# Performance work log

Hardware: AMD Instinct MI355X
Metric: run time of the kernel (lower is better)

The kernel has to match this reference:

```python
import jax, jax.numpy as jnp
import numpy as np
from math import sqrt

N_HEAD = 8
N_GROUPS = 32
EPS = 1e-5


def setup_inputs() -> dict:
    key = jax.random.key(0)
    k1, k2, k3 = jax.random.split(key, 3)
    B, C, T = 4, 256, 2048
    x = jax.random.normal(k1, (B, C, T), dtype=jnp.float32)
    gn_w = jnp.ones((C,), dtype=jnp.float32)
    gn_b = jnp.zeros((C,), dtype=jnp.float32)
    qkv_w = jax.random.normal(k2, (3 * C, C), dtype=jnp.float32) * (1.0 / sqrt(C))
    out_w = jax.random.normal(k3, (C, C), dtype=jnp.float32) * (1.0 / sqrt(C))
    out_b = jnp.zeros((C,), dtype=jnp.float32)
    return {"x": x, "gn_w": gn_w, "gn_b": gn_b, "qkv_w": qkv_w, "out_w": out_w, "out_b": out_b}


def reference(x, gn_w, gn_b, qkv_w, out_w, out_b):
    B, C, T = x.shape
    H = N_HEAD
    D = C // H
    # GroupNorm over (C//G, T) within each of G groups
    xg = x.reshape(B, N_GROUPS, -1)
    mu = jnp.mean(xg, axis=-1, keepdims=True)
    var = jnp.mean(jnp.square(xg - mu), axis=-1, keepdims=True)
    norm = ((xg - mu) * jax.lax.rsqrt(var + EPS)).reshape(B, C, T)
    norm = norm * gn_w[:, None] + gn_b[:, None]
    # 1x1 conv QKV projection (no bias)
    qkv = jnp.einsum('oc,bct->bot', qkv_w, norm)  # [B, 3C, T]
    qkv = qkv.reshape(B, H, 3 * D, T)
    q, k, v = jnp.split(qkv, 3, axis=2)  # each [B, H, D, T]
    # note: scale uses full channel count, matching the original module
    attn = jnp.einsum('bncl,bncx->bnlx', q, k) / sqrt(C)  # [B, H, T, T]
    attn = jax.nn.softmax(attn, axis=-1)
    out = jnp.einsum('bnlx,bncx->bncl', attn, v).reshape(B, C, T)
    # 1x1 conv out projection (with bias)
    out = jnp.einsum('oc,bct->bot', out_w, out) + out_b[:, None]
    return out + x
```

## Files before the change

kernel.cpp:

```cpp
#include <hip/hip_runtime.h>
#include <hip/hip_bf16.h>

#define B_ 4
#define C_ 256
#define T_ 2048
#define H_ 8

typedef __attribute__((ext_vector_type(8))) short short8;
typedef __attribute__((ext_vector_type(4))) float floatx4;
typedef __attribute__((ext_vector_type(16))) float floatx16;

static __device__ __forceinline__ float b2f(ushort u) {
  union { float f; unsigned v; } w; w.v = ((unsigned)u) << 16; return w.f;
}
static __device__ __forceinline__ ushort f2b(float f) {
  __hip_bfloat16 h = __float2bfloat16(f);
  return *reinterpret_cast<ushort*>(&h);
}

#define QWS_OFF   0
#define OWS_OFF   196608
#define OBS_OFF   262144
#define WCONV_N   262400
#define STATS_OFF 262400
#define NP_OFF    262912
#define QT_OFF    2360064
#define KT_OFF    4457216
#define VP_OFF    6554368
#define AT_OFF    8651520

__global__ __launch_bounds__(256) void prep_k(
    const void* __restrict__ xraw, const void* __restrict__ qw,
    const void* __restrict__ ow, const void* __restrict__ ob,
    const unsigned* __restrict__ gwraw, float* __restrict__ stats,
    ushort* __restrict__ ws)
{
  const bool f32 = (gwraw[0] == 0x3F800000u);
  const int tid = threadIdx.x;
  if (blockIdx.x >= 128) {
    const int idx = (blockIdx.x - 128) * 256 + tid;
    if (idx >= WCONV_N) return;
    if (idx < OWS_OFF) {
      const float v = f32 ? ((const float*)qw)[idx] : b2f(((const ushort*)qw)[idx]);
      const int o = idx >> 8, c = idx & 255;
      ws[QWS_OFF + ((size_t)(c >> 5) * 768 + o) * 32 + (c & 31)] = f2b(v);
    } else if (idx < OBS_OFF) {
      const int li = idx - OWS_OFF;
      const float v = f32 ? ((const float*)ow)[li] : b2f(((const ushort*)ow)[li]);
      const int o = li >> 8, c = li & 255;
      ws[OWS_OFF + ((size_t)(c >> 5) * 256 + o) * 32 + (c & 31)] = f2b(v);
    } else {
      const int li = idx - OBS_OFF;
      const float v = f32 ? ((const float*)ob)[li] : b2f(((const ushort*)ob)[li]);
      ws[OBS_OFF + li] = f2b(v);
    }
    return;
  }
  const int bg = blockIdx.x;
  const size_t base = (size_t)bg * 8 * T_;
  float s = 0.f, ss = 0.f;
  if (f32) {
    const float4* xv = (const float4*)((const float*)xraw + base);
    for (int i = tid; i < 4096; i += 256) {
      float4 u = xv[i];
      s += u.x + u.y + u.z + u.w;
      ss += u.x * u.x + u.y * u.y + u.z * u.z + u.w * u.w;
    }
  } else {
    const uint4* xv = (const uint4*)((const ushort*)xraw + base);
    for (int i = tid; i < 2048; i += 256) {
      uint4 u = xv[i];
      unsigned w4[4] = {u.x, u.y, u.z, u.w};
#pragma unroll
      for (int j = 0; j < 4; ++j) {
        float a = b2f((ushort)(w4[j] & 0xffff));
        float c = b2f((ushort)(w4[j] >> 16));
        s += a + c; ss += a * a + c * c;
      }
    }
  }
  __shared__ float sh[512];
  sh[tid] = s; sh[256 + tid] = ss;
  __syncthreads();
  for (int st = 128; st > 0; st >>= 1) {
    if (tid < st) { sh[tid] += sh[tid + st]; sh[256 + tid] += sh[256 + tid + st]; }
    __syncthreads();
  }
  if (tid == 0) {
    float mu = sh[0] * (1.f / 16384.f);
    float var = sh[256] * (1.f / 16384.f) - mu * mu;
    stats[bg * 2] = mu;
    stats[bg * 2 + 1] = rsqrtf(var + 1e-5f);
  }
}

__global__ __launch_bounds__(256) void gnapply_k(
    const void* __restrict__ xraw, const unsigned* __restrict__ gwraw,
    const void* __restrict__ gbraw, const float* __restrict__ stats,
    ushort* __restrict__ np)
{
  const bool f32 = (gwraw[0] == 0x3F800000u);
  const int t0 = blockIdx.x * 16, b = blockIdx.y;
  const int tid = threadIdx.x;
  __shared__ ushort lt[16][264];

  if (f32) {
    const int tl = tid & 15;
    const int cb = tid >> 4;
#pragma unroll
    for (int pass = 0; pass < 16; ++pass) {
      const int c = pass * 16 + cb;
      const int g = c >> 3;
      const float mu = stats[(b * 32 + g) * 2];
      const float rs = stats[(b * 32 + g) * 2 + 1];
      const float wv = ((const float*)gwraw)[c] * rs;
      const float bv = ((const float*)gbraw)[c] - mu * wv;
      const float xv = ((const float*)xraw)[((size_t)b * C_ + c) * T_ + t0 + tl];
      lt[tl][c] = f2b(xv * wv + bv);
    }
  } else {
    const int tl = (tid & 7) * 2;
    const int cb = tid >> 3;
#pragma unroll
    for (int pass = 0; pass < 8; ++pass) {
      const int c = pass * 32 + cb;
      const int g = c >> 3;
      const float mu = stats[(b * 32 + g) * 2];
      const float rs = stats[(b * 32 + g) * 2 + 1];
      const float wv = b2f(((const ushort*)gwraw)[c]) * rs;
      const float bv = b2f(((const ushort*)gbraw)[c]) - mu * wv;
      const unsigned u = *(const unsigned*)((const ushort*)xraw +
                          ((size_t)b * C_ + c) * T_ + t0 + tl);
      lt[tl][c]     = f2b(b2f((ushort)(u & 0xffff)) * wv + bv);
      lt[tl + 1][c] = f2b(b2f((ushort)(u >> 16)) * wv + bv);
    }
  }
  __syncthreads();
  {
    const int t = tid >> 4, ci = (tid & 15) * 8;
#pragma unroll
    for (int half = 0; half < 2; ++half) {
      const int c = half * 128 + ci;
      const int kp = c >> 5, co = c & 31;
      uint4 v = *(const uint4*)&lt[t][c];
      *(uint4*)(np + (((size_t)b * 8 + kp) * T_ + t0 + t) * 32 + co) = v;
    }
  }
}

__global__ __launch_bounds__(256) void qkvgemm_k(
    const ushort* __restrict__ qwp, const ushort* __restrict__ np,
    ushort* __restrict__ qt, ushort* __restrict__ kt, ushort* __restrict__ vP)
{
  const int b = blockIdx.z;
  const int m0 = blockIdx.x * 32;
  const int h = blockIdx.x / 3, sec = blockIdx.x % 3;
  const int tid = threadIdx.x;
  const int wave = tid >> 6, lane = tid & 63;
  const int qlane = lane & 15, quad = lane >> 4;
  const int tw0 = blockIdx.y * 128 + wave * 32;
  const float qscale = 0.0625f * 1.4426950408889634f;

  floatx4 acc[2][2] = {};
  if (sec < 2) {
#pragma unroll
    for (int k0 = 0; k0 < C_; k0 += 32) {
      const int kp = k0 >> 5;
      short8 af[2], bf[2];
#pragma unroll
      for (int mi = 0; mi < 2; ++mi)
        af[mi] = *(const short8*)(np + (((size_t)b * 8 + kp) * T_ + tw0 + mi * 16 + qlane) * 32 + quad * 8);
#pragma unroll
      for (int ni = 0; ni < 2; ++ni)
        bf[ni] = *(const short8*)(qwp + ((size_t)kp * 768 + m0 + ni * 16 + qlane) * 32 + quad * 8);
#pragma unroll
      for (int mi = 0; mi < 2; ++mi)
#pragma unroll
        for (int ni = 0; ni < 2; ++ni)
          acc[mi][ni] = __builtin_amdgcn_mfma_f32_16x16x32_bf16(af[mi], bf[ni], acc[mi][ni], 0, 0, 0);
    }
    const float sc = (sec == 0) ? qscale : 1.f;
    ushort* dst = ((sec == 0) ? qt : kt) + (size_t)(b * H_ + h) * T_ * 32;
#pragma unroll
    for (int mi = 0; mi < 2; ++mi)
#pragma unroll
      for (int ni = 0; ni < 2; ++ni)
#pragma unroll
        for (int r = 0; r < 4; ++r) {
          const int t = tw0 + mi * 16 + quad * 4 + r;
          const int d = ni * 16 + qlane;
          dst[(size_t)t * 32 + d] = f2b(acc[mi][ni][r] * sc);
        }
  } else {
#pragma unroll
    for (int k0 = 0; k0 < C_; k0 += 32) {
      const int kp = k0 >> 5;
      short8 af[2], bf[2];
#pragma unroll
      for (int mi = 0; mi < 2; ++mi)
        af[mi] = *(const short8*)(qwp + ((size_t)kp * 768 + m0 + mi * 16 + qlane) * 32 + quad * 8);
#pragma unroll
      for (int ni = 0; ni < 2; ++ni)
        bf[ni] = *(const short8*)(np + (((size_t)b * 8 + kp) * T_ + tw0 + ni * 16 + qlane) * 32 + quad * 8);
#pragma unroll
      for (int mi = 0; mi < 2; ++mi)
#pragma unroll
        for (int ni = 0; ni < 2; ++ni)
          acc[mi][ni] = __builtin_amdgcn_mfma_f32_16x16x32_bf16(af[mi], bf[ni], acc[mi][ni], 0, 0, 0);
    }
    ushort* dst = vP + (((size_t)(b * H_ + h) * 64 + (tw0 >> 5)) * 32) * 32;
#pragma unroll
    for (int mi = 0; mi < 2; ++mi)
#pragma unroll
      for (int ni = 0; ni < 2; ++ni)
#pragma unroll
        for (int r = 0; r < 4; ++r) {
          const int d = mi * 16 + quad * 4 + r;
          const int xi = ni * 16 + qlane;
          dst[(size_t)d * 32 + xi] = f2b(acc[mi][ni][r]);
        }
  }
}

__global__ __launch_bounds__(256) void attn_k(
    const ushort* __restrict__ qt, const ushort* __restrict__ kt,
    const ushort* __restrict__ vP, ushort* __restrict__ att)
{
  const int bh = blockIdx.y;
  const int tid = threadIdx.x;
  const int wave = tid >> 6, lane = tid & 63;
  const int qlane = lane & 15, quad = lane >> 4;
  const int l32 = lane & 31, hl = lane >> 5;
  const int l0 = blockIdx.x * 32;

  const ushort* qp = qt + (size_t)bh * T_ * 32;
  const ushort* kp = kt + (size_t)bh * T_ * 32;
  const ushort* vpp = vP + (size_t)bh * 64 * 32 * 32;

  __shared__ __align__(16) unsigned char blob[36864];
  ushort* pw0 = (ushort*)(blob + wave * 9216);
  float* cbo = (float*)blob;
  float* cbs = (float*)(blob + 18432);

  short8 qf0 = *(const short8*)(qp + (size_t)(l0 + l32) * 32 + hl * 8);
  short8 qf1 = *(const short8*)(qp + (size_t)(l0 + l32) * 32 + 16 + hl * 8);
  short8 ones;
#pragma unroll
  for (int j = 0; j < 8; ++j) ones[j] = (short)0x3F80;

  floatx4 o[2][2] = {};
  floatx4 os[2] = {};

  short8 kb[2][2][2], vb[2][2][2];
  {
    const int gx = wave * 64;
#pragma unroll
    for (int s = 0; s < 2; ++s)
#pragma unroll
      for (int dh = 0; dh < 2; ++dh)
        kb[0][s][dh] = *(const short8*)(kp + (size_t)(gx + s * 32 + l32) * 32 + dh * 16 + hl * 8);
#pragma unroll
    for (int dh = 0; dh < 2; ++dh)
#pragma unroll
      for (int xc = 0; xc < 2; ++xc)
        vb[0][dh][xc] = *(const short8*)(vpp + (((size_t)(gx >> 5) + xc) * 32 + dh * 16 + qlane) * 32 + quad * 8);
  }

  for (int i = 0; i < 8; ++i) {
    const int cur = i & 1, prv = cur ^ 1;
    ushort* pwr = pw0 + cur * 4608;
    ushort* prd = pw0 + prv * 4608;

    short8 pf[2][2];
    if (i > 0) {
      __asm__ volatile("s_waitcnt lgkmcnt(0)" ::: "memory");
#pragma unroll
      for (int lh = 0; lh < 2; ++lh)
#pragma unroll
        for (int xc = 0; xc < 2; ++xc)
          pf[lh][xc] = *(const short8*)(prd + (size_t)(lh * 16 + qlane) * 72 + xc * 32 + quad * 8);
    }

    floatx16 st0 = {}, st1 = {};
    st0 = __builtin_amdgcn_mfma_f32_32x32x16_bf16(kb[cur][0][0], qf0, st0, 0, 0, 0);
    st0 = __builtin_amdgcn_mfma_f32_32x32x16_bf16(kb[cur][0][1], qf1, st0, 0, 0, 0);
    st1 = __builtin_amdgcn_mfma_f32_32x32x16_bf16(kb[cur][1][0], qf0, st1, 0, 0, 0);
    st1 = __builtin_amdgcn_mfma_f32_32x32x16_bf16(kb[cur][1][1], qf1, st1, 0, 0, 0);

#pragma unroll
    for (int s = 0; s < 2; ++s) {
      const floatx16& stt = s ? st1 : st0;
#pragma unroll
      for (int rq = 0; rq < 4; ++rq) {
        unsigned u[4];
#pragma unroll
        for (int j = 0; j < 4; ++j)
          u[j] = __float_as_uint(__builtin_amdgcn_exp2f(stt[rq * 4 + j])) + 0x8000u;
        uint2 wpk;
        wpk.x = __builtin_amdgcn_perm(u[1], u[0], 0x07060302u);
        wpk.y = __builtin_amdgcn_perm(u[3], u[2], 0x07060302u);
        *(uint2*)(pwr + l32 * 72 + s * 32 + rq * 8 + hl * 4) = wpk;
      }
    }

    if (i > 0) {
#pragma unroll
      for (int lh = 0; lh < 2; ++lh)
#pragma unroll
        for (int xc = 0; xc < 2; ++xc) {
          o[lh][0] = __builtin_amdgcn_mfma_f32_16x16x32_bf16(pf[lh][xc], vb[prv][0][xc], o[lh][0], 0, 0, 0);
          o[lh][1] = __builtin_amdgcn_mfma_f32_16x16x32_bf16(pf[lh][xc], vb[prv][1][xc], o[lh][1], 0, 0, 0);
          os[lh] = __builtin_amdgcn_mfma_f32_16x16x32_bf16(pf[lh][xc], ones, os[lh], 0, 0, 0);
        }
    }

    {
      const int gxn = wave * 64 + (((i + 1) & 7) << 8);
#pragma unroll
      for (int s = 0; s < 2; ++s)
#pragma unroll
        for (int dh = 0; dh < 2; ++dh)
          kb[prv][s][dh] = *(const short8*)(kp + (size_t)(gxn + s * 32 + l32) * 32 + dh * 16 + hl * 8);
#pragma unroll
      for (int dh = 0; dh < 2; ++dh)
#pragma unroll
        for (int xc = 0; xc < 2; ++xc)
          vb[prv][dh][xc] = *(const short8*)(vpp + (((size_t)(gxn >> 5) + xc) * 32 + dh * 16 + qlane) * 32 + quad * 8);
    }
  }

  {
    __asm__ volatile("s_waitcnt lgkmcnt(0)" ::: "memory");
    ushort* prd = pw0 + 4608;
#pragma unroll
    for (int lh = 0; lh < 2; ++lh)
#pragma unroll
      for (int xc = 0; xc < 2; ++xc) {
        short8 pf = *(const short8*)(prd + (size_t)(lh * 16 + qlane) * 72 + xc * 32 + quad * 8);
        o[lh][0] = __builtin_amdgcn_mfma_f32_16x16x32_bf16(pf, vb[1][0][xc], o[lh][0], 0, 0, 0);
        o[lh][1] = __builtin_amdgcn_mfma_f32_16x16x32_bf16(pf, vb[1][1][xc], o[lh][1], 0, 0, 0);
        os[lh] = __builtin_amdgcn_mfma_f32_16x16x32_bf16(pf, ones, os[lh], 0, 0, 0);
      }
  }

  __syncthreads();
#pragma unroll
  for (int lh = 0; lh < 2; ++lh)
#pragma unroll
    for (int dh = 0; dh < 2; ++dh)
#pragma unroll
      for (int r = 0; r < 4; ++r)
        cbo[((size_t)wave * 32 + lh * 16 + quad * 4 + r) * 36 + dh * 16 + qlane] = o[lh][dh][r];
  if (qlane == 0) {
#pragma unroll
    for (int lh = 0; lh < 2; ++lh)
#pragma unroll
      for (int r = 0; r < 4; ++r)
        cbs[wave * 32 + lh * 16 + quad * 4 + r] = os[lh][r];
  }
  __syncthreads();

  {
    const int l = tid >> 3, dq = (tid & 7) * 4;
    float a4[4] = {0.f, 0.f, 0.f, 0.f};
    float ssum = 0.f;
#pragma unroll
    for (int w = 0; w < 4; ++w) {
      ssum += cbs[w * 32 + l];
#pragma unroll
      for (int j = 0; j < 4; ++j) a4[j] += cbo[((size_t)w * 32 + l) * 36 + dq + j];
    }
    const float inv = 1.f / ssum;
    uint2 wpk;
    wpk.x = (unsigned)f2b(a4[0] * inv) | ((unsigned)f2b(a4[1] * inv) << 16);
    wpk.y = (unsigned)f2b(a4[2] * inv) | ((unsigned)f2b(a4[3] * inv) << 16);
    *(uint2*)(att + ((size_t)bh * T_ + l0 + l) * 32 + dq) = wpk;
  }
}

__global__ __launch_bounds__(256) void outgemm_k(
    const ushort* __restrict__ owp, const ushort* __restrict__ att,
    const ushort* __restrict__ bias, const void* __restrict__ xraw,
    const unsigned* __restrict__ gwraw, void* __restrict__ out)
{
  const bool f32 = (gwraw[0] == 0x3F800000u);
  const int b = blockIdx.z;
  const int m0 = blockIdx.x * 32;
  const int tid = threadIdx.x;
  const int wave = tid >> 6, lane = tid & 63;
  const int qlane = lane & 15, quad = lane >> 4;
  const int tw0 = blockIdx.y * 128 + wave * 32;

  floatx4 acc[2][2] = {};
#pragma unroll
  for (int k0 = 0; k0 < C_; k0 += 32) {
    const int kp = k0 >> 5;
    short8 af[2], bf[2];
#pragma unroll
    for (int mi = 0; mi < 2; ++mi)
      af[mi] = *(const short8*)(owp + ((size_t)kp * 256 + m0 + mi * 16 + qlane) * 32 + quad * 8);
#pragma unroll
    for (int ni = 0; ni < 2; ++ni)
      bf[ni] = *(const short8*)(att + (((size_t)b * 8 + kp) * T_ + tw0 + ni * 16 + qlane) * 32 + quad * 8);
#pragma unroll
    for (int mi = 0; mi < 2; ++mi)
#pragma unroll
      for (int ni = 0; ni < 2; ++ni)
        acc[mi][ni] = __builtin_amdgcn_mfma_f32_16x16x32_bf16(af[mi], bf[ni], acc[mi][ni], 0, 0, 0);
  }

#pragma unroll
  for (int mi = 0; mi < 2; ++mi) {
#pragma unroll
    for (int ni = 0; ni < 2; ++ni) {
#pragma unroll
      for (int r = 0; r < 4; ++r) {
        const int row = m0 + mi * 16 + quad * 4 + r;
        const int col = tw0 + ni * 16 + qlane;
        const size_t off = (size_t)b * C_ * T_ + (size_t)row * T_ + col;
        float v = acc[mi][ni][r] + b2f(bias[row]);
        if (f32) {
          v += ((const float*)xraw)[off];
          ((float*)out)[off] = v;
        } else {
          v += b2f(((const ushort*)xraw)[off]);
          ((ushort*)out)[off] = f2b(v);
        }
      }
    }
  }
}

extern "C" void kernel_launch(void* const* d_in, const int* in_sizes, int n_in,
                              void* d_out, int out_size, void* d_ws, size_t ws_size,
                              hipStream_t stream) {
  const void* xraw  = d_in[0];
  const unsigned* gwraw = (const unsigned*)d_in[1];
  const void* gbraw = d_in[2];
  const void* qwraw = d_in[3];
  const void* owraw = d_in[4];
  const void* obraw = d_in[5];

  ushort* ws = (ushort*)d_ws;
  ushort* qwp = ws + QWS_OFF;
  ushort* owp = ws + OWS_OFF;
  ushort* obs = ws + OBS_OFF;
  float*  stats = (float*)(ws + STATS_OFF);
  ushort* np  = ws + NP_OFF;
  ushort* qtb = ws + QT_OFF;
  ushort* ktb = ws + KT_OFF;
  ushort* vPb = ws + VP_OFF;
  ushort* att = ws + AT_OFF;

  prep_k<<<dim3(128 + (WCONV_N + 255) / 256), 256, 0, stream>>>(
      xraw, qwraw, owraw, obraw, gwraw, stats, ws);

  gnapply_k<<<dim3(T_ / 16, B_), 256, 0, stream>>>(
      xraw, gwraw, gbraw, stats, np);

  qkvgemm_k<<<dim3(24, T_ / 128, B_), 256, 0, stream>>>(
      qwp, np, qtb, ktb, vPb);

  attn_k<<<dim3(T_ / 32, B_ * H_), 256, 0, stream>>>(qtb, ktb, vPb, att);

  outgemm_k<<<dim3(C_ / 32, T_ / 128, B_), 256, 0, stream>>>(
      owp, att, obs, xraw, gwraw, d_out);
}
```

Measured before the change: 136.6 us.

## Keep softmax probabilities in registers as MFMA operand, drop LDS round-trip

```diff
diff --git a/kernel.cpp b/kernel.cpp
--- a/kernel.cpp
+++ b/kernel.cpp
@@ -229,7 +229,6 @@
   const int bh = blockIdx.y;
   const int tid = threadIdx.x;
   const int wave = tid >> 6, lane = tid & 63;
-  const int qlane = lane & 15, quad = lane >> 4;
   const int l32 = lane & 31, hl = lane >> 5;
   const int l0 = blockIdx.x * 32;
 
@@ -237,49 +236,38 @@
   const ushort* kp = kt + (size_t)bh * T_ * 32;
   const ushort* vpp = vP + (size_t)bh * 64 * 32 * 32;
 
-  __shared__ __align__(16) unsigned char blob[36864];
-  ushort* pw0 = (ushort*)(blob + wave * 9216);
-  float* cbo = (float*)blob;
-  float* cbs = (float*)(blob + 18432);
+  __shared__ float cbo[4][32][33];
+  __shared__ float cbs[4][64];
 
   short8 qf0 = *(const short8*)(qp + (size_t)(l0 + l32) * 32 + hl * 8);
   short8 qf1 = *(const short8*)(qp + (size_t)(l0 + l32) * 32 + 16 + hl * 8);
-  short8 ones;
-#pragma unroll
-  for (int j = 0; j < 8; ++j) ones[j] = (short)0x3F80;
-
-  floatx4 o[2][2] = {};
-  floatx4 os[2] = {};
-
-  short8 kb[2][2][2], vb[2][2][2];
+
+  floatx16 o = {};
+  float rsum = 0.f;
+
+  short8 kb[2][2][2];
+  short8 va[2][2][2];
   {
     const int gx = wave * 64;
 #pragma unroll
-    for (int s = 0; s < 2; ++s)
+    for (int s = 0; s < 2; ++s) {
 #pragma unroll
       for (int dh = 0; dh < 2; ++dh)
         kb[0][s][dh] = *(const short8*)(kp + (size_t)(gx + s * 32 + l32) * 32 + dh * 16 + hl * 8);
 #pragma unroll
-    for (int dh = 0; dh < 2; ++dh)
-#pragma unroll
-      for (int xc = 0; xc < 2; ++xc)
-        vb[0][dh][xc] = *(const short8*)(vpp + (((size_t)(gx >> 5) + xc) * 32 + dh * 16 + qlane) * 32 + quad * 8);
+      for (int ks = 0; ks < 2; ++ks) {
+        const ushort* vrow = vpp + ((size_t)((gx >> 5) + s) * 32 + l32) * 32;
+        uint2 lo = *(const uint2*)(vrow + ks * 16 + 4 * hl);
+        uint2 hi = *(const uint2*)(vrow + ks * 16 + 8 + 4 * hl);
+        union { unsigned u[4]; short8 v; } pk;
+        pk.u[0] = lo.x; pk.u[1] = lo.y; pk.u[2] = hi.x; pk.u[3] = hi.y;
+        va[0][s][ks] = pk.v;
+      }
+    }
   }
 
   for (int i = 0; i < 8; ++i) {
-    const int cur = i & 1, prv = cur ^ 1;
-    ushort* pwr = pw0 + cur * 4608;
-    ushort* prd = pw0 + prv * 4608;
-
-    short8 pf[2][2];
-    if (i > 0) {
-      __asm__ volatile("s_waitcnt lgkmcnt(0)" ::: "memory");
-#pragma unroll
-      for (int lh = 0; lh < 2; ++lh)
-#pragma unroll
-        for (int xc = 0; xc < 2; ++xc)
-          pf[lh][xc] = *(const short8*)(prd + (size_t)(lh * 16 + qlane) * 72 + xc * 32 + quad * 8);
-    }
+    const int cur = i & 1, nxt = cur ^ 1;
 
     floatx16 st0 = {}, st1 = {};
     st0 = __builtin_amdgcn_mfma_f32_32x32x16_bf16(kb[cur][0][0], qf0, st0, 0, 0, 0);
@@ -287,88 +275,65 @@
     st1 = __builtin_amdgcn_mfma_f32_32x32x16_bf16(kb[cur][1][0], qf0, st1, 0, 0, 0);
     st1 = __builtin_amdgcn_mfma_f32_32x32x16_bf16(kb[cur][1][1], qf1, st1, 0, 0, 0);
 
+    {
+      const int gxn = wave * 64 + (((i + 1) & 7) << 8);
+#pragma unroll
+      for (int s = 0; s < 2; ++s) {
+#pragma unroll
+        for (int dh = 0; dh < 2; ++dh)
+          kb[nxt][s][dh] = *(const short8*)(kp + (size_t)(gxn + s * 32 + l32) * 32 + dh * 16 + hl * 8);
+#pragma unroll
+        for (int ks = 0; ks < 2; ++ks) {
+          const ushort* vrow = vpp + ((size_t)((gxn >> 5) + s) * 32 + l32) * 32;
+          uint2 lo = *(const uint2*)(vrow + ks * 16 + 4 * hl);
+          uint2 hi = *(const uint2*)(vrow + ks * 16 + 8 + 4 * hl);
+          union { unsigned u[4]; short8 v; } pk;
+          pk.u[0] = lo.x; pk.u[1] = lo.y; pk.u[2] = hi.x; pk.u[3] = hi.y;
+          va[nxt][s][ks] = pk.v;
+        }
+      }
+    }
+
 #pragma unroll
     for (int s = 0; s < 2; ++s) {
       const floatx16& stt = s ? st1 : st0;
-#pragma unroll
-      for (int rq = 0; rq < 4; ++rq) {
-        unsigned u[4];
-#pragma unroll
-        for (int j = 0; j < 4; ++j)
-          u[j] = __float_as_uint(__builtin_amdgcn_exp2f(stt[rq * 4 + j])) + 0x8000u;
-        uint2 wpk;
-        wpk.x = __builtin_amdgcn_perm(u[1], u[0], 0x07060302u);
-        wpk.y = __builtin_amdgcn_perm(u[3], u[2], 0x07060302u);
-        *(uint2*)(pwr + l32 * 72 + s * 32 + rq * 8 + hl * 4) = wpk;
-      }
-    }
-
-    if (i > 0) {
-#pragma unroll
-      for (int lh = 0; lh < 2; ++lh)
-#pragma unroll
-        for (int xc = 0; xc < 2; ++xc) {
-          o[lh][0] = __builtin_amdgcn_mfma_f32_16x16x32_bf16(pf[lh][xc], vb[prv][0][xc], o[lh][0], 0, 0, 0);
-          o[lh][1] = __builtin_amdgcn_mfma_f32_16x16x32_bf16(pf[lh][xc], vb[prv][1][xc], o[lh][1], 0, 0, 0);
-          os[lh] = __builtin_amdgcn_mfma_f32_16x16x32_bf16(pf[lh][xc], ones, os[lh], 0, 0, 0);
-        }
-    }
-
-    {
-      const int gxn = wave * 64 + (((i + 1) & 7) << 8);
-#pragma unroll
-      for (int s = 0; s < 2; ++s)
-#pragma unroll
-        for (int dh = 0; dh < 2; ++dh)
-          kb[prv][s][dh] = *(const short8*)(kp + (size_t)(gxn + s * 32 + l32) * 32 + dh * 16 + hl * 8);
-#pragma unroll
-      for (int dh = 0; dh < 2; ++dh)
-#pragma unroll
-        for (int xc = 0; xc < 2; ++xc)
-          vb[prv][dh][xc] = *(const short8*)(vpp + (((size_t)(gxn >> 5) + xc) * 32 + dh * 16 + qlane) * 32 + quad * 8);
-    }
-  }
-
-  {
-    __asm__ volatile("s_waitcnt lgkmcnt(0)" ::: "memory");
-    ushort* prd = pw0 + 4608;
-#pragma unroll
-    for (int lh = 0; lh < 2; ++lh)
-#pragma unroll
-      for (int xc = 0; xc < 2; ++xc) {
-        short8 pf = *(const short8*)(prd + (size_t)(lh * 16 + qlane) * 72 + xc * 32 + quad * 8);
-        o[lh][0] = __builtin_amdgcn_mfma_f32_16x16x32_bf16(pf, vb[1][0][xc], o[lh][0], 0, 0, 0);
-        o[lh][1] = __builtin_amdgcn_mfma_f32_16x16x32_bf16(pf, vb[1][1][xc], o[lh][1], 0, 0, 0);
-        os[lh] = __builtin_amdgcn_mfma_f32_16x16x32_bf16(pf, ones, os[lh], 0, 0, 0);
-      }
-  }
-
-  __syncthreads();
-#pragma unroll
-  for (int lh = 0; lh < 2; ++lh)
-#pragma unroll
-    for (int dh = 0; dh < 2; ++dh)
-#pragma unroll
-      for (int r = 0; r < 4; ++r)
-        cbo[((size_t)wave * 32 + lh * 16 + quad * 4 + r) * 36 + dh * 16 + qlane] = o[lh][dh][r];
-  if (qlane == 0) {
-#pragma unroll
-    for (int lh = 0; lh < 2; ++lh)
-#pragma unroll
-      for (int r = 0; r < 4; ++r)
-        cbs[wave * 32 + lh * 16 + quad * 4 + r] = os[lh][r];
-  }
+      unsigned w[8];
+#pragma unroll
+      for (int p = 0; p < 8; ++p) {
+        const float e0 = __builtin_amdgcn_exp2f(stt[2 * p]);
+        const float e1 = __builtin_amdgcn_exp2f(stt[2 * p + 1]);
+        rsum += e0 + e1;
+        const unsigned u0 = __float_as_uint(e0) + 0x8000u;
+        const unsigned u1 = __float_as_uint(e1) + 0x8000u;
+        w[p] = __builtin_amdgcn_perm(u1, u0, 0x07060302u);
+      }
+#pragma unroll
+      for (int ks = 0; ks < 2; ++ks) {
+        union { unsigned u[4]; short8 v; } pf;
+        pf.u[0] = w[ks * 4 + 0]; pf.u[1] = w[ks * 4 + 1];
+        pf.u[2] = w[ks * 4 + 2]; pf.u[3] = w[ks * 4 + 3];
+        o = __builtin_amdgcn_mfma_f32_32x32x16_bf16(va[cur][s][ks], pf.v, o, 0, 0, 0);
+      }
+    }
+  }
+
+#pragma unroll
+  for (int r = 0; r < 16; ++r) {
+    const int d = 4 * hl + (r & 3) + 8 * (r >> 2);
+    cbo[wave][d][l32] = o[r];
+  }
+  cbs[wave][hl * 32 + l32] = rsum;
   __syncthreads();
 
   {
     const int l = tid >> 3, dq = (tid & 7) * 4;
+    float ssum = 0.f;
     float a4[4] = {0.f, 0.f, 0.f, 0.f};
-    float ssum = 0.f;
 #pragma unroll
     for (int w = 0; w < 4; ++w) {
-      ssum += cbs[w * 32 + l];
-#pragma unroll
-      for (int j = 0; j < 4; ++j) a4[j] += cbo[((size_t)w * 32 + l) * 36 + dq + j];
+      ssum += cbs[w][l] + cbs[w][32 + l];
+#pragma unroll
+      for (int j = 0; j < 4; ++j) a4[j] += cbo[w][dq + j][l];
     }
     const float inv = 1.f / ssum;
     uint2 wpk;
```

After: 149.7 us. 9.6% more time.
